# Performance work log

Measured on AMD Instinct MI355X. Metric: run time of the kernel, lower is better.

## Reference

```python
import jax, jax.numpy as jnp
import numpy as np

D_MODEL = 256
NHEAD = 8
AGG = 4
NPE = (832.0, 832.0, 832.0, 832.0)
LAYER_NAMES = ['self', 'cross'] * 4


def layer_norm(x, g, b, eps=1e-5):
    mu = x.mean(-1, keepdims=True)
    var = ((x - mu) ** 2).mean(-1, keepdims=True)
    return (x - mu) * jax.lax.rsqrt(var + eps) * g + b


def rope_tables(h, w, d_model=D_MODEL):
    # i/j positions start at 1 (torch cumsum of ones); npe train/test scaling
    i = (jnp.arange(1, h + 1, dtype=jnp.float32) * (NPE[0] / NPE[2]))[:, None, None]
    j = (jnp.arange(1, w + 1, dtype=jnp.float32) * (NPE[1] / NPE[3]))[None, :, None]
    d4 = d_model // 4
    div = jnp.exp(jnp.arange(d4, dtype=jnp.float32) * (-np.log(10000.0) / d4))

    def interleave(a, bb):
        a = jnp.broadcast_to(a, (h, w, d4))
        bb = jnp.broadcast_to(bb, (h, w, d4))
        return jnp.stack([a, bb], -1).reshape(h, w, 2 * d4)

    sin = interleave(jnp.sin(i * div), jnp.sin(j * div))
    cos = interleave(jnp.cos(i * div), jnp.cos(j * div))
    return jnp.repeat(sin, 2, axis=-1), jnp.repeat(cos, 2, axis=-1)  # [h,w,d_model]


def rotate_half(x):
    xp = x.reshape(*x.shape[:-1], -1, 2)
    return jnp.stack([-xp[..., 1], xp[..., 0]], -1).reshape(*x.shape)


def apply_rope(x, sin, cos):  # x: [b,h,w,c]
    return x * cos + rotate_half(x) * sin


def encoder_layer(x, source, p, use_rope):
    bs, C, H0, W0 = x.shape
    # depthwise-conv aggregation of query features (stride=kernel=AGG, no bias)
    q = jax.lax.conv_general_dilated(
        x, p['agg_w'], (AGG, AGG), 'VALID',
        dimension_numbers=('NCHW', 'OIHW', 'NCHW'), feature_group_count=C)
    q = layer_norm(q.transpose(0, 2, 3, 1), p['ln1_g'], p['ln1_b'])  # [b,h,w,C]
    # max-pool aggregation of source features
    s = jax.lax.reduce_window(source, -jnp.inf, jax.lax.max,
                              (1, 1, AGG, AGG), (1, 1, AGG, AGG), 'VALID')
    s = layer_norm(s.transpose(0, 2, 3, 1), p['ln1_g'], p['ln1_b'])
    query = q @ p['qw']
    key = s @ p['kw']
    value = s @ p['vw']
    if use_rope:
        sin_q, cos_q = rope_tables(query.shape[1], query.shape[2])
        query = apply_rope(query, sin_q, cos_q)
        sin_k, cos_k = rope_tables(key.shape[1], key.shape[2])
        key = apply_rope(key, sin_k, cos_k)
    L = query.shape[1] * query.shape[2]
    S = key.shape[1] * key.shape[2]
    dh = C // NHEAD
    qh = query.reshape(bs, L, NHEAD, dh)
    kh = key.reshape(bs, S, NHEAD, dh)
    vh = value.reshape(bs, S, NHEAD, dh)
    scores = jnp.einsum('blhd,bshd->bhls', qh, kh) / jnp.asarray(dh, qh.dtype) ** 0.5
    attn = jax.nn.softmax(scores, axis=-1)
    m = jnp.einsum('bhls,bshd->blhd', attn, vh).reshape(bs, L, C)
    m = m @ p['mw']  # merge
    m = m.reshape(bs, H0 // AGG, W0 // AGG, C).transpose(0, 3, 1, 2)
    # bilinear upsample x4, align_corners=False (half-pixel, matches jax.image)
    m = jax.image.resize(m, (bs, C, H0, W0), method='bilinear')
    cat = jnp.concatenate([x, m], axis=1).transpose(0, 2, 3, 1)  # [b,H,W,2C]
    h1 = cat @ p['w1']
    h1 = jnp.where(h1 >= 0, h1, 0.01 * h1)  # LeakyReLU
    out = layer_norm(h1 @ p['w2'], p['ln2_g'], p['ln2_b']).transpose(0, 3, 1, 2)
    return x + out


def _forward(feat0, feat1, params):
    for i, name in enumerate(LAYER_NAMES):
        p = {k: v[i] for k, v in params.items()}
        if name == 'self':
            feat0 = encoder_layer(feat0, feat0, p, use_rope=True)
            feat1 = encoder_layer(feat1, feat1, p, use_rope=True)
        else:
            feat0 = encoder_layer(feat0, feat1, p, use_rope=False)
            feat1 = encoder_layer(feat1, feat0, p, use_rope=False)
    return feat0, feat1


def setup_inputs() -> dict:
    key = jax.random.key(0)
    ks = jax.random.split(key, 10)
    C = D_MODEL
    NL = len(LAYER_NAMES)

    def xavier(k, shape, fan_in, fan_out):
        return jax.random.normal(k, shape, jnp.float32) * np.sqrt(2.0 / (fan_in + fan_out))

    return {
        'feat0': jax.random.normal(ks[0], (2, C, 96, 96), jnp.float32),
        'feat1': jax.random.normal(ks[1], (2, C, 96, 96), jnp.float32),
        'agg_w': jax.random.normal(ks[2], (NL, C, 1, AGG, AGG), jnp.float32) * 0.1,
        'qw': xavier(ks[3], (NL, C, C), C, C),
        'kw': xavier(ks[4], (NL, C, C), C, C),
        'vw': xavier(ks[5], (NL, C, C), C, C),
        'mw': xavier(ks[6], (NL, C, C), C, C),
        'w1': xavier(ks[7], (NL, 2 * C, 2 * C), 2 * C, 2 * C),
        'w2': xavier(ks[8], (NL, 2 * C, C), 2 * C, C),
        'ln1_g': jnp.ones((NL, C), jnp.float32),
        'ln1_b': jnp.zeros((NL, C), jnp.float32),
        'ln2_g': jnp.ones((NL, C), jnp.float32),
        'ln2_b': jnp.zeros((NL, C), jnp.float32),
    }


def reference(feat0, feat1, agg_w, qw, kw, vw, mw, w1, w2, ln1_g, ln1_b, ln2_g, ln2_b):
    params = dict(agg_w=agg_w, qw=qw, kw=kw, vw=vw, mw=mw, w1=w1, w2=w2,
                  ln1_g=ln1_g, ln1_b=ln1_b, ln2_g=ln2_g, ln2_b=ln2_b)
    return _forward(feat0, feat1, params)
```

## Files before the change

kernel.cpp:

```cpp
#include <hip/hip_runtime.h>
#include <math.h>

constexpr int BSZ = 2;
constexpr int CH  = 256;
constexpr int IH  = 96, IW = 96;
constexpr int HSS = 24, WSS = 24;
constexpr int SL  = HSS * WSS;
constexpr int NHD = 8, DHD = 32;
constexpr int CH2 = 512;
constexpr int PIX = IH * IW;
constexpr int MFFN = BSZ * PIX;
constexpr long FEATN = (long)BSZ * PIX * CH;

typedef __attribute__((ext_vector_type(8))) short bf16x8;
typedef __attribute__((ext_vector_type(4))) float f32x4;
typedef _Float16 f16;
typedef __attribute__((ext_vector_type(8))) _Float16 f16x8;
typedef __attribute__((ext_vector_type(4))) _Float16 f16x4;


__device__ inline unsigned short f2bf(float f) {
  unsigned u = __float_as_uint(f);
  u += 0x7FFFu + ((u >> 16) & 1u);
  return (unsigned short)(u >> 16);
}
__device__ inline float bf2f(unsigned short u) {
  return __uint_as_float((unsigned)u << 16);
}

__device__ inline void gload16(const void* g, void* l) {
  __builtin_amdgcn_global_load_lds(
      (const __attribute__((address_space(1))) unsigned int*)g,
      (__attribute__((address_space(3))) unsigned int*)l, 16, 0, 0);
}

__global__ __launch_bounds__(256) void k_in_tr(const float* __restrict__ in,
                                               float* __restrict__ out,
                                               unsigned short* __restrict__ outb) {
  __shared__ float t[32][33];
  const int b = blockIdx.z;
  const int p0 = blockIdx.x * 32, c0 = blockIdx.y * 32;
  const int tx = threadIdx.x & 31, ty = threadIdx.x >> 5;
#pragma unroll
  for (int r = 0; r < 4; ++r)
    t[tx][ty + r * 8] = in[((long)b * CH + c0 + ty + r * 8) * PIX + p0 + tx];
  __syncthreads();
#pragma unroll
  for (int r = 0; r < 4; ++r) {
    float v = t[ty + r * 8][tx];
    long row = (long)b * PIX + p0 + ty + r * 8;
    out[row * CH + c0 + tx] = v;
    outb[row * CH + ((c0 + tx) ^ (ty << 3))] = f2bf(v);
  }
}

__global__ __launch_bounds__(256) void k_out_tr(const float* __restrict__ in,
                                                float* __restrict__ out) {
  __shared__ float t[32][33];
  const int b = blockIdx.z;
  const int p0 = blockIdx.x * 32, c0 = blockIdx.y * 32;
  const int tx = threadIdx.x & 31, ty = threadIdx.x >> 5;
#pragma unroll
  for (int r = 0; r < 4; ++r)
    t[ty + r * 8][tx] = in[((long)b * PIX + p0 + ty + r * 8) * CH + c0 + tx];
  __syncthreads();
#pragma unroll
  for (int r = 0; r < 4; ++r)
    out[((long)b * CH + c0 + ty + r * 8) * PIX + p0 + tx] = t[tx][ty + r * 8];
}

__global__ __launch_bounds__(256) void k_wt(const float* __restrict__ W,
                                            unsigned short* __restrict__ WT,
                                            int K, int N, long strideW, long strideT) {
  const long z = blockIdx.z;
  W  += z * strideW;
  WT += z * strideT;
  __shared__ float t[32][33];
  const int n0 = blockIdx.x * 32, k0 = blockIdx.y * 32;
  const int tx = threadIdx.x & 31, ty = threadIdx.x >> 5;
#pragma unroll
  for (int r = 0; r < 4; ++r)
    t[ty + r * 8][tx] = W[(long)(k0 + ty + r * 8) * N + n0 + tx];
  __syncthreads();
#pragma unroll
  for (int r = 0; r < 4; ++r) {
    int n = n0 + ty + r * 8;
    WT[(long)n * K + ((k0 + tx) ^ ((n & 7) << 3))] = f2bf(t[tx][ty + r * 8]);
  }
}

__global__ __launch_bounds__(256) void k_cvt(const float* __restrict__ W,
                                             unsigned short* __restrict__ O) {
  const int i = blockIdx.x;
  const long z = blockIdx.y;
  const int k = threadIdx.x;
  O[(z * CH + i) * CH + (k ^ ((i & 7) << 3))] = f2bf(W[(z * CH + i) * CH + k]);
}

__global__ __launch_bounds__(256) void k_rope_tables(float* __restrict__ sinT,
                                                     float* __restrict__ cosT) {
  int l = blockIdx.x;
  int d = threadIdx.x;
  int ii = l / WSS + 1;
  int jj = l % WSS + 1;
  int kidx = d >> 2;
  bool is_i = ((d >> 1) & 1) == 0;
  float div = expf((float)kidx * -0.14391156831212787f);
  float pos = is_i ? (float)ii : (float)jj;
  float ang = pos * div;
  sinT[(long)l * CH + d] = sinf(ang);
  cosT[(long)l * CH + d] = cosf(ang);
}

__global__ __launch_bounds__(256) void k_agg(const unsigned short* __restrict__ x,
                                             const unsigned short* __restrict__ src,
                                             const float* __restrict__ aggw,
                                             const float* __restrict__ g,
                                             const float* __restrict__ bt,
                                             unsigned short* __restrict__ qln,
                                             unsigned short* __restrict__ sln,
                                             int nb) {
  int bi = blockIdx.x;
  int mode = 0;
  if (bi >= nb * SL) { mode = 1; bi -= nb * SL; }
  int b = bi / SL, l = bi % SL;
  int i = l / WSS, j = l % WSS;
  int c = threadIdx.x;
  const unsigned short* in = mode ? src : x;
  float v;
  if (mode == 0) {
    v = 0.f;
#pragma unroll
    for (int r = 0; r < 4; ++r)
#pragma unroll
      for (int s = 0; s < 4; ++s)
        v += bf2f(in[(((long)b * IH + i * 4 + r) * IW + j * 4 + s) * CH +
                     (c ^ (((j * 4 + s) & 7) << 3))]) *
             aggw[c * 16 + r * 4 + s];
  } else {
    v = -INFINITY;
#pragma unroll
    for (int r = 0; r < 4; ++r)
#pragma unroll
      for (int s = 0; s < 4; ++s)
        v = fmaxf(v, bf2f(in[(((long)b * IH + i * 4 + r) * IW + j * 4 + s) * CH +
                             (c ^ (((j * 4 + s) & 7) << 3))]));
  }
  __shared__ float red[8];
  float s1 = v, s2 = v * v;
#pragma unroll
  for (int d = 1; d < 64; d <<= 1) { s1 += __shfl_xor(s1, d); s2 += __shfl_xor(s2, d); }
  int wv = threadIdx.x >> 6;
  if ((threadIdx.x & 63) == 0) { red[wv * 2] = s1; red[wv * 2 + 1] = s2; }
  __syncthreads();
  s1 = red[0] + red[2] + red[4] + red[6];
  s2 = red[1] + red[3] + red[5] + red[7];
  float mu = s1 * (1.f / CH);
  float var = s2 * (1.f / CH) - mu * mu;
  float o = (v - mu) * rsqrtf(var + 1e-5f) * g[c] + bt[c];
  (mode ? sln : qln)[(long)(b * SL + l) * CH + (c ^ ((l & 7) << 3))] = f2bf(o);
}

template <int BM, int BN, int OUT>
__global__ __launch_bounds__(256) void k_mm(const unsigned short* __restrict__ A,
                                            const unsigned short* __restrict__ A2,
                                            const unsigned short* __restrict__ Bt,
                                            void* __restrict__ C0, void* __restrict__ C1,
                                            void* __restrict__ C2,
                                            int M, int K, int lda, int ldb,
                                            int koffA, int koffB, int ldc,
                                            const float* __restrict__ sinT,
                                            const float* __restrict__ cosT,
                                            long zsA, long zsB, long zsC) {
  constexpr int BK = 64;
  constexpr int WM = BM / 2, WN = BN / 2;
  constexpr int FM = WM / 16, FN = WN / 16;
  constexpr int RA = BM * BK / 2048, RB = BN * BK / 2048;
  __shared__ unsigned short As[2][BM * BK];
  __shared__ unsigned short Bs[2][BN * BK];
  const int tid = threadIdx.x;
  const int lane = tid & 63, w = tid >> 6;
  const int wr = w >> 1, wc = w & 1;
  const int lq = lane & 15, g = lane >> 4;
  const int sw = (lq & 7) << 3;
  const int bm = blockIdx.x * BM, bn = blockIdx.y * BN;
  const long z = blockIdx.z;
  const unsigned short* Ap = ((OUT == 4 && bn >= CH) ? A2 : A) + z * zsA + koffA;
  const unsigned short* Bp = Bt + z * zsB + koffB;

  auto stA = [&](int buf, int k0) {
#pragma unroll
    for (int i = 0; i < RA; ++i) {
      int e = (i * 256 + tid) * 8;
      gload16(Ap + (size_t)(bm + (e >> 6)) * lda + k0 + (e & 63), &As[buf][e]);
    }
  };
  auto stB = [&](int buf, int k0) {
#pragma unroll
    for (int i = 0; i < RB; ++i) {
      int e = (i * 256 + tid) * 8;
      gload16(Bp + (size_t)(bn + (e >> 6)) * ldb + k0 + (e & 63), &Bs[buf][e]);
    }
  };

  f32x4 acc[FM][FN] = {};
  stA(0, 0); stB(0, 0);
  asm volatile("s_waitcnt vmcnt(0)" ::: "memory");
  __syncthreads();
  int cur = 0;
  for (int k0 = 0; k0 < K; k0 += BK) {
    if (k0 + BK < K) { stA(cur ^ 1, k0 + BK); stB(cur ^ 1, k0 + BK); }
#pragma unroll
    for (int ks = 0; ks < 2; ++ks) {
      const int kx = (ks * 32 + g * 8) ^ sw;
      bf16x8 a[FM], b[FN];
#pragma unroll
      for (int m = 0; m < FM; ++m)
        a[m] = *(const bf16x8*)&As[cur][(wr * WM + m * 16 + lq) * BK + kx];
#pragma unroll
      for (int n = 0; n < FN; ++n)
        b[n] = *(const bf16x8*)&Bs[cur][(wc * WN + n * 16 + lq) * BK + kx];
#pragma unroll
      for (int m = 0; m < FM; ++m)
#pragma unroll
        for (int n = 0; n < FN; ++n)
          acc[m][n] = __builtin_amdgcn_mfma_f32_16x16x32_bf16(a[m], b[n], acc[m][n], 0, 0, 0);
    }
    __syncthreads();
    cur ^= 1;
  }
#pragma unroll
  for (int m = 0; m < FM; ++m) {
    const int rowb = bm + wr * WM + m * 16 + g * 4;
#pragma unroll
    for (int n = 0; n < FN; ++n) {
      const int col = bn + wc * WN + n * 16 + lq;
#pragma unroll
      for (int r = 0; r < 4; ++r) {
        const int row = rowb + r;
        float v = acc[m][n][r];
        if (OUT == 0) {
          ((float*)C0 + z * zsC)[(size_t)row * ldc + col] = v;
        } else if (OUT == 5) {
          ((unsigned short*)C0 + z * zsC)[(size_t)row * ldc + (col ^ ((row & 7) << 3))] = f2bf(v);
        } else {
          const int b = row / SL, s = row - b * SL;
          const int which = col >> 8;
          const int ch = col & 255;
          float vp = __shfl_xor(v, 1);
          if (which < 2 && sinT) {
            float sn = sinT[(size_t)s * CH + ch];
            float cs = cosT[(size_t)s * CH + ch];
            v = ((lane & 1) == 0) ? v * cs - vp * sn : v * cs + vp * sn;
          }
          if (which == 0) v *= 0.17677669529663687f;
          const int h = ch >> 5, d = ch & 31;
          if (which == 0)
            ((f16*)C0)[(((size_t)b * NHD + h) * SL + s) * DHD + d] = (f16)v;
          else if (which == 1)
            ((f16*)C1)[(((size_t)b * NHD + h) * SL + s) * DHD + d] = (f16)v;
          else
            ((f16*)C2)[(((size_t)b * NHD + h) * DHD + d) * SL + s] = (f16)v;
        }
      }
    }
  }
}

__global__ __launch_bounds__(64) void k_attn(const f16* __restrict__ qh,
                                             const f16* __restrict__ kh,
                                             const f16* __restrict__ vt,
                                             unsigned short* __restrict__ msgA) {
  const int bh = blockIdx.x;
  const int b = bh >> 3, h = bh & 7;
  const int lane = threadIdx.x;
  const int lq = lane & 15, g = lane >> 4;
  const int q0 = blockIdx.y * 16;

  const f16x8 qf = *(const f16x8*)&qh[((size_t)bh * SL + q0 + lq) * DHD + g * 8];
  const f16* kbase = kh + (size_t)bh * SL * DHD;
  const f16* vbase = vt + (size_t)bh * DHD * SL;

  f16x8 kf = *(const f16x8*)&kbase[(size_t)lq * DHD + g * 8];
  f16x4 va = *(const f16x4*)&vbase[(size_t)lq * SL + g * 4];
  f16x4 vb = *(const f16x4*)&vbase[(size_t)(16 + lq) * SL + g * 4];

  f32x4 o0 = {}, o1 = {};
  float m = -1e30f, l = 0.f;
  for (int t = 0; t < 36; ++t) {
    const int tn = t < 35 ? t + 1 : 35;
    f16x8 kfn = *(const f16x8*)&kbase[((size_t)(tn * 16 + lq)) * DHD + g * 8];
    f16x4 van = *(const f16x4*)&vbase[(size_t)lq * SL + tn * 16 + g * 4];
    f16x4 vbn = *(const f16x4*)&vbase[(size_t)(16 + lq) * SL + tn * 16 + g * 4];
    f32x4 s = __builtin_amdgcn_mfma_f32_16x16x32_f16(kf, qf, (f32x4){0.f, 0.f, 0.f, 0.f}, 0, 0, 0);
    float tm = fmaxf(fmaxf(s[0], s[1]), fmaxf(s[2], s[3]));
    tm = fmaxf(tm, __shfl_xor(tm, 16));
    tm = fmaxf(tm, __shfl_xor(tm, 32));
    if (__any(tm > m + 5.f)) {
      float mn = fmaxf(m, tm);
      float f = __expf(m - mn);
      o0 *= f; o1 *= f; l *= f; m = mn;
    }
    float e0 = __expf(s[0] - m), e1 = __expf(s[1] - m);
    float e2 = __expf(s[2] - m), e3 = __expf(s[3] - m);
    l += (e0 + e1) + (e2 + e3);
    f16x4 ef = {(f16)e0, (f16)e1, (f16)e2, (f16)e3};
    o0 = __builtin_amdgcn_mfma_f32_16x16x16f16(va, ef, o0, 0, 0, 0);
    o1 = __builtin_amdgcn_mfma_f32_16x16x16f16(vb, ef, o1, 0, 0, 0);
    kf = kfn; va = van; vb = vbn;
  }
  l += __shfl_xor(l, 16);
  l += __shfl_xor(l, 32);
  float inv = 1.f / l;
  const int swz = (lq & 7) << 3;
  unsigned short* mrow = msgA + ((size_t)(b * SL + q0 + lq)) * CH;
#pragma unroll
  for (int mt = 0; mt < 2; ++mt) {
    f32x4 o = mt ? o1 : o0;
    unsigned a0 = f2bf(o[0] * inv) | ((unsigned)f2bf(o[1] * inv) << 16);
    unsigned a1 = f2bf(o[2] * inv) | ((unsigned)f2bf(o[3] * inv) << 16);
    uint2 u; u.x = a0; u.y = a1;
    *(uint2*)&mrow[(h * DHD + mt * 16 + g * 4) ^ swz] = u;
  }
}

__global__ __launch_bounds__(256) void k_ffn1(const unsigned short* __restrict__ xb,
                                              const unsigned short* __restrict__ w1T,
                                              const float* __restrict__ Z,
                                              unsigned short* __restrict__ h1) {
  constexpr int BM = 64, BN = 128, BK = 64, K = 256;
  constexpr int WM = 32, WN = 64, FM = 2, FN = 4;
  __shared__ unsigned short As[2][BM * BK];
  __shared__ unsigned short Bs[BN * BK];
  const int tid = threadIdx.x;
  const int lane = tid & 63, w = tid >> 6;
  const int wr = w >> 1, wc = w & 1;
  const int lq = lane & 15, g = lane >> 4;
  const int sw = (lq & 7) << 3;
  const int bm = blockIdx.x * BM, bn = blockIdx.y * BN;

  auto stA = [&](int buf, int k0) {
#pragma unroll
    for (int i = 0; i < 2; ++i) {
      int e = (i * 256 + tid) * 8;
      gload16(xb + (size_t)(bm + (e >> 6)) * 256 + k0 + (e & 63), &As[buf][e]);
    }
  };
  auto stB = [&](int k0) {
#pragma unroll
    for (int i = 0; i < 4; ++i) {
      int e = (i * 256 + tid) * 8;
      gload16(w1T + (size_t)(bn + (e >> 6)) * 512 + k0 + (e & 63), &Bs[e]);
    }
  };

  f32x4 acc[FM][FN] = {};
  stA(0, 0); stB(0);
  asm volatile("s_waitcnt vmcnt(0)" ::: "memory");
  __syncthreads();
  int cur = 0;
  for (int k0 = 0; k0 < K; k0 += BK) {
    if (k0 + BK < K) stA(cur ^ 1, k0 + BK);
#pragma unroll
    for (int ks = 0; ks < 2; ++ks) {
      const int kx = (ks * 32 + g * 8) ^ sw;
      bf16x8 a[FM], b[FN];
#pragma unroll
      for (int m = 0; m < FM; ++m)
        a[m] = *(const bf16x8*)&As[cur][(wr * WM + m * 16 + lq) * BK + kx];
#pragma unroll
      for (int n = 0; n < FN; ++n)
        b[n] = *(const bf16x8*)&Bs[(wc * WN + n * 16 + lq) * BK + kx];
#pragma unroll
      for (int m = 0; m < FM; ++m)
#pragma unroll
        for (int n = 0; n < FN; ++n)
          acc[m][n] = __builtin_amdgcn_mfma_f32_16x16x32_bf16(a[m], b[n], acc[m][n], 0, 0, 0);
    }
    __syncthreads();
    if (k0 + BK < K) stB(k0 + BK);
    asm volatile("s_waitcnt vmcnt(0)" ::: "memory");
    __syncthreads();
    cur ^= 1;
  }
#pragma unroll
  for (int m = 0; m < FM; ++m) {
    const int rowb = bm + wr * WM + m * 16 + g * 4;
#pragma unroll
    for (int r = 0; r < 4; ++r) {
      const int row = rowb + r;
      const int b = row / PIX;
      const int p = row - b * PIX;
      const int y = p / IW, xx = p - y * IW;
      float sy = (y + 0.5f) * 0.25f - 0.5f;
      float sx = (xx + 0.5f) * 0.25f - 0.5f;
      int y0 = (int)floorf(sy); float wy = sy - y0;
      int x0 = (int)floorf(sx); float wx = sx - x0;
      int y1 = min(y0 + 1, HSS - 1); y0 = max(y0, 0);
      int x1 = min(x0 + 1, WSS - 1); x0 = max(x0, 0);
      const float* Zb = Z + (size_t)b * SL * CH2;
      const float* z00 = Zb + (size_t)(y0 * WSS + x0) * CH2;
      const float* z01 = Zb + (size_t)(y0 * WSS + x1) * CH2;
      const float* z10 = Zb + (size_t)(y1 * WSS + x0) * CH2;
      const float* z11 = Zb + (size_t)(y1 * WSS + x1) * CH2;
      float w00 = (1.f - wy) * (1.f - wx), w01 = (1.f - wy) * wx;
      float w10 = wy * (1.f - wx), w11 = wy * wx;
      const int rs = (row & 7) << 3;
#pragma unroll
      for (int n = 0; n < FN; ++n) {
        const int col = bn + wc * WN + n * 16 + lq;
        float v = acc[m][n][r] + w00 * z00[col] + w01 * z01[col] +
                  w10 * z10[col] + w11 * z11[col];
        v = v >= 0.f ? v : 0.01f * v;
        h1[(size_t)row * CH2 + (col ^ rs)] = f2bf(v);
      }
    }
  }
}

__global__ __launch_bounds__(256) void k_ffn2(const unsigned short* __restrict__ A,
                                              const unsigned short* __restrict__ Bt,
                                              const float* __restrict__ g2,
                                              const float* __restrict__ b2,
                                              float* __restrict__ x,
                                              unsigned short* __restrict__ xb) {
  constexpr int BM = 32, BK = 64, K = 512;
  __shared__ unsigned short As[2][BM * BK];
  __shared__ unsigned short Bs[256 * BK];
  __shared__ float sS[2][BM], sQ[2][BM];
  __shared__ float gS[256], bS[256];
  const int tid = threadIdx.x;
  const int lane = tid & 63, w = tid >> 6;
  const int wr = w >> 1, wc = w & 1;
  const int lq = lane & 15, g = lane >> 4;
  const int sw = (lq & 7) << 3;
  const int bm = blockIdx.x * BM;
  gS[tid] = g2[tid]; bS[tid] = b2[tid];

  auto stA = [&](int buf, int k0) {
    int e = tid * 8;
    gload16(A + (size_t)(bm + (e >> 6)) * K + k0 + (e & 63), &As[buf][e]);
  };
  auto stB = [&](int k0) {
#pragma unroll
    for (int i = 0; i < 8; ++i) {
      int e = (i * 256 + tid) * 8;
      gload16(Bt + (size_t)(e >> 6) * K + k0 + (e & 63), &Bs[e]);
    }
  };

  f32x4 acc[8] = {};
  stA(0, 0); stB(0);
  asm volatile("s_waitcnt vmcnt(0)" ::: "memory");
  __syncthreads();
  int cur = 0;
  for (int k0 = 0; k0 < K; k0 += BK) {
    if (k0 + BK < K) stA(cur ^ 1, k0 + BK);
#pragma unroll
    for (int ks = 0; ks < 2; ++ks) {
      const int kx = (ks * 32 + g * 8) ^ sw;
      bf16x8 a = *(const bf16x8*)&As[cur][(wr * 16 + lq) * BK + kx];
      bf16x8 b[8];
#pragma unroll
      for (int n = 0; n < 8; ++n)
        b[n] = *(const bf16x8*)&Bs[(wc * 128 + n * 16 + lq) * BK + kx];
#pragma unroll
      for (int n = 0; n < 8; ++n)
        acc[n] = __builtin_amdgcn_mfma_f32_16x16x32_bf16(a, b[n], acc[n], 0, 0, 0);
    }
    __syncthreads();
    if (k0 + BK < K) stB(k0 + BK);
    asm volatile("s_waitcnt vmcnt(0)" ::: "memory");
    __syncthreads();
    cur ^= 1;
  }
#pragma unroll
  for (int r = 0; r < 4; ++r) {
    float s1 = 0.f, s2 = 0.f;
#pragma unroll
    for (int n = 0; n < 8; ++n) {
      float v = acc[n][r];
      s1 += v; s2 += v * v;
    }
#pragma unroll
    for (int d = 1; d < 16; d <<= 1) {
      s1 += __shfl_xor(s1, d);
      s2 += __shfl_xor(s2, d);
    }
    if (lq == 0) {
      int row = wr * 16 + g * 4 + r;
      sS[wc][row] = s1; sQ[wc][row] = s2;
    }
  }
  __syncthreads();
#pragma unroll
  for (int r = 0; r < 4; ++r) {
    int row = wr * 16 + g * 4 + r;
    float mu = (sS[0][row] + sS[1][row]) * (1.f / CH);
    float var = (sQ[0][row] + sQ[1][row]) * (1.f / CH) - mu * mu;
    float rs = rsqrtf(var + 1e-5f);
    size_t gr = (size_t)(bm + row) * CH;
    const int swr = ((bm + row) & 7) << 3;
#pragma unroll
    for (int n = 0; n < 8; ++n) {
      int col = wc * 128 + n * 16 + lq;
      float o = (acc[n][r] - mu) * rs * gS[col] + bS[col];
      float nx = x[gr + col] + o;
      x[gr + col] = nx;
      xb[gr + (col ^ swr)] = f2bf(nx);
    }
  }
}

struct LayerP {
  const float *aggw, *g1, *b1, *g2, *b2;
  const unsigned short *qkvT, *w1T, *w2T, *wcT;
};

struct Bufs {
  unsigned short *qln, *sln, *msgA, *h1, *xb;
  f16 *qh, *kh, *vt;
  float *Zbuf, *f;
  const float *sinT, *cosT;
};

static void attn_part(long xoff, long soff, const LayerP& p, bool rope, int nb,
                      const Bufs& B, hipStream_t stream) {
  const int M = nb * SL;
  k_agg<<<dim3(2 * nb * SL), 256, 0, stream>>>(B.xb + xoff, B.xb + soff, p.aggw,
                                               p.g1, p.b1, B.qln, B.sln, nb);
  const float* sT = rope ? B.sinT : nullptr;
  const float* cT = rope ? B.cosT : nullptr;
  k_mm<32, 64, 4><<<dim3(M / 32, 12), 256, 0, stream>>>(
      B.qln, B.sln, p.qkvT, B.qh, B.kh, B.vt, M, CH, CH, CH, 0, 0, 0, sT, cT, 0, 0, 0);
  k_attn<<<dim3(nb * NHD, 36), 64, 0, stream>>>(B.qh, B.kh, B.vt, B.msgA);
  k_mm<64, 64, 0><<<dim3(M / 64, 8), 256, 0, stream>>>(
      B.msgA, nullptr, p.wcT, B.Zbuf, nullptr, nullptr, M, CH, CH, CH, 0, 0, CH2,
      nullptr, nullptr, 0, 0, 0);
}

static void ffn_part(int fi, int nf, const float* Zs, const LayerP& p, const Bufs& B,
                     hipStream_t stream) {
  const int M = nf * MFFN;
  k_ffn1<<<dim3(M / 64, CH2 / 128), 256, 0, stream>>>(B.xb + (long)fi * FEATN, p.w1T, Zs, B.h1);
  k_ffn2<<<dim3(M / 32), 256, 0, stream>>>(B.h1, p.w2T, p.g2, p.b2,
                                           B.f + (long)fi * FEATN, B.xb + (long)fi * FEATN);
}

extern "C" void kernel_launch(void* const* d_in, const int* in_sizes, int n_in,
                              void* d_out, int out_size, void* d_ws, size_t ws_size,
                              hipStream_t stream) {
  const float* in_f0 = (const float*)d_in[0];
  const float* in_f1 = (const float*)d_in[1];
  const float* aggw  = (const float*)d_in[2];
  const float* qw    = (const float*)d_in[3];
  const float* kw    = (const float*)d_in[4];
  const float* vw    = (const float*)d_in[5];
  const float* mw    = (const float*)d_in[6];
  const float* w1    = (const float*)d_in[7];
  const float* w2    = (const float*)d_in[8];
  const float* g1    = (const float*)d_in[9];
  const float* b1    = (const float*)d_in[10];
  const float* g2    = (const float*)d_in[11];
  const float* b2    = (const float*)d_in[12];
  (void)in_sizes; (void)n_in; (void)out_size; (void)ws_size;

  char* cur = (char*)d_ws;
  auto alloc = [&](size_t bytes) { void* p = cur; cur += (bytes + 255) & ~(size_t)255; return p; };
  float*          f    = (float*)alloc((size_t)2 * FEATN * 4);
  unsigned short* xb   = (unsigned short*)alloc((size_t)2 * FEATN * 2);
  unsigned short* h1   = (unsigned short*)alloc((size_t)2 * MFFN * CH2 * 2);
  float*          Zbuf = (float*)alloc((size_t)4 * SL * CH2 * 4);
  unsigned short* msgA = (unsigned short*)alloc((size_t)4 * SL * CH * 2);
  unsigned short* qln  = (unsigned short*)alloc((size_t)4 * SL * CH * 2);
  unsigned short* sln  = (unsigned short*)alloc((size_t)4 * SL * CH * 2);
  f16* qh = (f16*)alloc((size_t)4 * NHD * SL * DHD * 2);
  f16* kh = (f16*)alloc((size_t)4 * NHD * SL * DHD * 2);
  f16* vt = (f16*)alloc((size_t)4 * NHD * SL * DHD * 2);
  float* sinT = (float*)alloc((size_t)SL * CH * 4);
  float* cosT = (float*)alloc((size_t)SL * CH * 4);
  unsigned short* qkvT = (unsigned short*)alloc((size_t)8 * 3 * CH * CH * 2);
  unsigned short* mwB  = (unsigned short*)alloc((size_t)8 * CH * CH * 2);
  unsigned short* w1T  = (unsigned short*)alloc((size_t)8 * CH2 * CH2 * 2);
  unsigned short* w2T  = (unsigned short*)alloc((size_t)8 * CH * CH2 * 2);
  unsigned short* wcT  = (unsigned short*)alloc((size_t)8 * CH2 * CH * 2);

  k_in_tr<<<dim3(PIX / 32, CH / 32, BSZ), 256, 0, stream>>>(in_f0, f, xb);
  k_in_tr<<<dim3(PIX / 32, CH / 32, BSZ), 256, 0, stream>>>(in_f1, f + FEATN, xb + FEATN);
  k_rope_tables<<<dim3(SL), 256, 0, stream>>>(sinT, cosT);
  k_wt<<<dim3(CH / 32, CH / 32, 8), 256, 0, stream>>>(qw, qkvT, CH, CH, (long)CH * CH, (long)3 * CH * CH);
  k_wt<<<dim3(CH / 32, CH / 32, 8), 256, 0, stream>>>(kw, qkvT + (size_t)CH * CH, CH, CH, (long)CH * CH, (long)3 * CH * CH);
  k_wt<<<dim3(CH / 32, CH / 32, 8), 256, 0, stream>>>(vw, qkvT + (size_t)2 * CH * CH, CH, CH, (long)CH * CH, (long)3 * CH * CH);
  k_cvt<<<dim3(CH, 8), 256, 0, stream>>>(mw, mwB);
  k_wt<<<dim3(CH2 / 32, CH2 / 32, 8), 256, 0, stream>>>(w1, w1T, CH2, CH2, (long)CH2 * CH2, (long)CH2 * CH2);
  k_wt<<<dim3(CH / 32, CH2 / 32, 8), 256, 0, stream>>>(w2, w2T, CH2, CH, (long)CH2 * CH, (long)CH * CH2);
  k_mm<64, 64, 5><<<dim3(CH2 / 64, CH / 64, 8), 256, 0, stream>>>(
      w1T, nullptr, mwB, wcT, nullptr, nullptr, CH2, CH, CH2, CH, 256, 0, CH,
      nullptr, nullptr, (long)CH2 * CH2, (long)CH * CH, (long)CH2 * CH);

  Bufs B{qln, sln, msgA, h1, xb, qh, kh, vt, Zbuf, f, sinT, cosT};

  for (int i = 0; i < 8; ++i) {
    LayerP p{aggw + (long)i * CH * 16,
             g1 + i * CH, b1 + i * CH, g2 + i * CH, b2 + i * CH,
             qkvT + (long)i * 3 * CH * CH,
             w1T + (long)i * CH2 * CH2, w2T + (long)i * CH * CH2,
             wcT + (long)i * CH2 * CH};
    if ((i & 1) == 0) {
      attn_part(0, 0, p, true, 4, B, stream);
      ffn_part(0, 2, Zbuf, p, B, stream);
    } else {
      attn_part(0, FEATN, p, false, 2, B, stream);
      ffn_part(0, 1, Zbuf, p, B, stream);
      attn_part(FEATN, 0, p, false, 2, B, stream);
      ffn_part(1, 1, Zbuf, p, B, stream);
    }
  }

  float* outp = (float*)d_out;
  k_out_tr<<<dim3(PIX / 32, CH / 32, BSZ), 256, 0, stream>>>(f, outp);
  k_out_tr<<<dim3(PIX / 32, CH / 32, BSZ), 256, 0, stream>>>(f + FEATN, outp + FEATN);
}
```

Before: 1.028 ms.

## Split attention keys across two waves and enlarge FFN GEMM row tiles

The attention kernel now runs two wavefronts per block, each handling half of the key tiles, and merges their partial softmax max, sum and outputs through shared memory. This halves the serial loop length per query tile. Separately, the FFN1 and FFN2 GEMMs double their row tile (64→128 and 32→64) so each weight tile loaded into shared memory is reused over more rows. The larger tiles use more LDS and registers per block and produce fewer blocks, which may reduce occupancy.

```diff
diff --git a/kernel.cpp b/kernel.cpp
--- a/kernel.cpp
+++ b/kernel.cpp
@@ -267,28 +267,32 @@
   }
 }
 
-__global__ __launch_bounds__(64) void k_attn(const f16* __restrict__ qh,
-                                             const f16* __restrict__ kh,
-                                             const f16* __restrict__ vt,
-                                             unsigned short* __restrict__ msgA) {
+__global__ __launch_bounds__(128) void k_attn(const f16* __restrict__ qh,
+                                              const f16* __restrict__ kh,
+                                              const f16* __restrict__ vt,
+                                              unsigned short* __restrict__ msgA) {
   const int bh = blockIdx.x;
   const int b = bh >> 3, h = bh & 7;
-  const int lane = threadIdx.x;
+  const int tid = threadIdx.x;
+  const int sid = tid >> 6;
+  const int lane = tid & 63;
   const int lq = lane & 15, g = lane >> 4;
   const int q0 = blockIdx.y * 16;
 
   const f16x8 qf = *(const f16x8*)&qh[((size_t)bh * SL + q0 + lq) * DHD + g * 8];
   const f16* kbase = kh + (size_t)bh * SL * DHD;
   const f16* vbase = vt + (size_t)bh * DHD * SL;
-
-  f16x8 kf = *(const f16x8*)&kbase[(size_t)lq * DHD + g * 8];
-  f16x4 va = *(const f16x4*)&vbase[(size_t)lq * SL + g * 4];
-  f16x4 vb = *(const f16x4*)&vbase[(size_t)(16 + lq) * SL + g * 4];
+  const int t0 = sid * 18;
+
+  f16x8 kf = *(const f16x8*)&kbase[((size_t)(t0 * 16 + lq)) * DHD + g * 8];
+  f16x4 va = *(const f16x4*)&vbase[(size_t)lq * SL + t0 * 16 + g * 4];
+  f16x4 vb = *(const f16x4*)&vbase[(size_t)(16 + lq) * SL + t0 * 16 + g * 4];
 
   f32x4 o0 = {}, o1 = {};
   float m = -1e30f, l = 0.f;
-  for (int t = 0; t < 36; ++t) {
-    const int tn = t < 35 ? t + 1 : 35;
+  for (int tt = 0; tt < 18; ++tt) {
+    const int t = t0 + tt;
+    const int tn = tt < 17 ? t + 1 : t;
     f16x8 kfn = *(const f16x8*)&kbase[((size_t)(tn * 16 + lq)) * DHD + g * 8];
     f16x4 van = *(const f16x4*)&vbase[(size_t)lq * SL + tn * 16 + g * 4];
     f16x4 vbn = *(const f16x4*)&vbase[(size_t)(16 + lq) * SL + tn * 16 + g * 4];
@@ -311,25 +315,39 @@
   }
   l += __shfl_xor(l, 16);
   l += __shfl_xor(l, 32);
-  float inv = 1.f / l;
+
+  __shared__ float mS[2][16], lS[2][16];
+  __shared__ float oS[2][2][16][17];
+  if (g == 0) { mS[sid][lq] = m; lS[sid][lq] = l; }
+#pragma unroll
+  for (int r = 0; r < 4; ++r) {
+    oS[sid][0][g * 4 + r][lq] = o0[r];
+    oS[sid][1][g * 4 + r][lq] = o1[r];
+  }
+  __syncthreads();
+  float m0 = mS[0][lq], m1 = mS[1][lq];
+  float l0 = lS[0][lq], l1 = lS[1][lq];
+  float mn = fmaxf(m0, m1);
+  float f0 = __expf(m0 - mn), f1 = __expf(m1 - mn);
+  float inv = 1.f / (l0 * f0 + l1 * f1);
+  float ov[4];
+#pragma unroll
+  for (int r = 0; r < 4; ++r)
+    ov[r] = (oS[0][sid][g * 4 + r][lq] * f0 + oS[1][sid][g * 4 + r][lq] * f1) * inv;
   const int swz = (lq & 7) << 3;
   unsigned short* mrow = msgA + ((size_t)(b * SL + q0 + lq)) * CH;
-#pragma unroll
-  for (int mt = 0; mt < 2; ++mt) {
-    f32x4 o = mt ? o1 : o0;
-    unsigned a0 = f2bf(o[0] * inv) | ((unsigned)f2bf(o[1] * inv) << 16);
-    unsigned a1 = f2bf(o[2] * inv) | ((unsigned)f2bf(o[3] * inv) << 16);
-    uint2 u; u.x = a0; u.y = a1;
-    *(uint2*)&mrow[(h * DHD + mt * 16 + g * 4) ^ swz] = u;
-  }
+  unsigned a0 = f2bf(ov[0]) | ((unsigned)f2bf(ov[1]) << 16);
+  unsigned a1 = f2bf(ov[2]) | ((unsigned)f2bf(ov[3]) << 16);
+  uint2 u; u.x = a0; u.y = a1;
+  *(uint2*)&mrow[(h * DHD + sid * 16 + g * 4) ^ swz] = u;
 }
 
 __global__ __launch_bounds__(256) void k_ffn1(const unsigned short* __restrict__ xb,
                                               const unsigned short* __restrict__ w1T,
                                               const float* __restrict__ Z,
                                               unsigned short* __restrict__ h1) {
-  constexpr int BM = 64, BN = 128, BK = 64, K = 256;
-  constexpr int WM = 32, WN = 64, FM = 2, FN = 4;
+  constexpr int BM = 128, BN = 128, BK = 64, K = 256;
+  constexpr int WM = 64, WN = 64, FM = 4, FN = 4;
   __shared__ unsigned short As[2][BM * BK];
   __shared__ unsigned short Bs[BN * BK];
   const int tid = threadIdx.x;
@@ -341,7 +359,7 @@
 
   auto stA = [&](int buf, int k0) {
 #pragma unroll
-    for (int i = 0; i < 2; ++i) {
+    for (int i = 0; i < 4; ++i) {
       int e = (i * 256 + tid) * 8;
       gload16(xb + (size_t)(bm + (e >> 6)) * 256 + k0 + (e & 63), &As[buf][e]);
     }
@@ -424,7 +442,8 @@
                                               const float* __restrict__ b2,
                                               float* __restrict__ x,
                                               unsigned short* __restrict__ xb) {
-  constexpr int BM = 32, BK = 64, K = 512;
+  constexpr int BM = 64, BK = 64, K = 512;
+  constexpr int WM = 32, FM = 2;
   __shared__ unsigned short As[2][BM * BK];
   __shared__ unsigned short Bs[256 * BK];
   __shared__ float sS[2][BM], sQ[2][BM];
@@ -438,8 +457,11 @@
   gS[tid] = g2[tid]; bS[tid] = b2[tid];
 
   auto stA = [&](int buf, int k0) {
-    int e = tid * 8;
-    gload16(A + (size_t)(bm + (e >> 6)) * K + k0 + (e & 63), &As[buf][e]);
+#pragma unroll
+    for (int i = 0; i < 2; ++i) {
+      int e = (i * 256 + tid) * 8;
+      gload16(A + (size_t)(bm + (e >> 6)) * K + k0 + (e & 63), &As[buf][e]);
+    }
   };
   auto stB = [&](int k0) {
 #pragma unroll
@@ -449,7 +471,7 @@
     }
   };
 
-  f32x4 acc[8] = {};
+  f32x4 acc[FM][8] = {};
   stA(0, 0); stB(0);
   asm volatile("s_waitcnt vmcnt(0)" ::: "memory");
   __syncthreads();
@@ -459,14 +481,19 @@
 #pragma unroll
     for (int ks = 0; ks < 2; ++ks) {
       const int kx = (ks * 32 + g * 8) ^ sw;
-      bf16x8 a = *(const bf16x8*)&As[cur][(wr * 16 + lq) * BK + kx];
+      bf16x8 a[FM];
+#pragma unroll
+      for (int m = 0; m < FM; ++m)
+        a[m] = *(const bf16x8*)&As[cur][(wr * WM + m * 16 + lq) * BK + kx];
       bf16x8 b[8];
 #pragma unroll
       for (int n = 0; n < 8; ++n)
         b[n] = *(const bf16x8*)&Bs[(wc * 128 + n * 16 + lq) * BK + kx];
 #pragma unroll
-      for (int n = 0; n < 8; ++n)
-        acc[n] = __builtin_amdgcn_mfma_f32_16x16x32_bf16(a, b[n], acc[n], 0, 0, 0);
+      for (int m = 0; m < FM; ++m)
+#pragma unroll
+        for (int n = 0; n < 8; ++n)
+          acc[m][n] = __builtin_amdgcn_mfma_f32_16x16x32_bf16(a[m], b[n], acc[m][n], 0, 0, 0);
     }
     __syncthreads();
     if (k0 + BK < K) stB(k0 + BK);
@@ -475,41 +502,45 @@
     cur ^= 1;
   }
 #pragma unroll
-  for (int r = 0; r < 4; ++r) {
-    float s1 = 0.f, s2 = 0.f;
-#pragma unroll
-    for (int n = 0; n < 8; ++n) {
-      float v = acc[n][r];
-      s1 += v; s2 += v * v;
-    }
-#pragma unroll
-    for (int d = 1; d < 16; d <<= 1) {
-      s1 += __shfl_xor(s1, d);
-      s2 += __shfl_xor(s2, d);
-    }
-    if (lq == 0) {
-      int row = wr * 16 + g * 4 + r;
-      sS[wc][row] = s1; sQ[wc][row] = s2;
-    }
-  }
-  __syncthreads();
-#pragma unroll
-  for (int r = 0; r < 4; ++r) {
-    int row = wr * 16 + g * 4 + r;
-    float mu = (sS[0][row] + sS[1][row]) * (1.f / CH);
-    float var = (sQ[0][row] + sQ[1][row]) * (1.f / CH) - mu * mu;
-    float rs = rsqrtf(var + 1e-5f);
-    size_t gr = (size_t)(bm + row) * CH;
-    const int swr = ((bm + row) & 7) << 3;
-#pragma unroll
-    for (int n = 0; n < 8; ++n) {
-      int col = wc * 128 + n * 16 + lq;
-      float o = (acc[n][r] - mu) * rs * gS[col] + bS[col];
-      float nx = x[gr + col] + o;
-      x[gr + col] = nx;
-      xb[gr + (col ^ swr)] = f2bf(nx);
-    }
-  }
+  for (int m = 0; m < FM; ++m)
+#pragma unroll
+    for (int r = 0; r < 4; ++r) {
+      float s1 = 0.f, s2 = 0.f;
+#pragma unroll
+      for (int n = 0; n < 8; ++n) {
+        float v = acc[m][n][r];
+        s1 += v; s2 += v * v;
+      }
+#pragma unroll
+      for (int d = 1; d < 16; d <<= 1) {
+        s1 += __shfl_xor(s1, d);
+        s2 += __shfl_xor(s2, d);
+      }
+      if (lq == 0) {
+        int row = wr * WM + m * 16 + g * 4 + r;
+        sS[wc][row] = s1; sQ[wc][row] = s2;
+      }
+    }
+  __syncthreads();
+#pragma unroll
+  for (int m = 0; m < FM; ++m)
+#pragma unroll
+    for (int r = 0; r < 4; ++r) {
+      int row = wr * WM + m * 16 + g * 4 + r;
+      float mu = (sS[0][row] + sS[1][row]) * (1.f / CH);
+      float var = (sQ[0][row] + sQ[1][row]) * (1.f / CH) - mu * mu;
+      float rs = rsqrtf(var + 1e-5f);
+      size_t gr = (size_t)(bm + row) * CH;
+      const int swr = ((bm + row) & 7) << 3;
+#pragma unroll
+      for (int n = 0; n < 8; ++n) {
+        int col = wc * 128 + n * 16 + lq;
+        float o = (acc[m][n][r] - mu) * rs * gS[col] + bS[col];
+        float nx = x[gr + col] + o;
+        x[gr + col] = nx;
+        xb[gr + (col ^ swr)] = f2bf(nx);
+      }
+    }
 }
 
 struct LayerP {
@@ -533,7 +564,7 @@
   const float* cT = rope ? B.cosT : nullptr;
   k_mm<32, 64, 4><<<dim3(M / 32, 12), 256, 0, stream>>>(
       B.qln, B.sln, p.qkvT, B.qh, B.kh, B.vt, M, CH, CH, CH, 0, 0, 0, sT, cT, 0, 0, 0);
-  k_attn<<<dim3(nb * NHD, 36), 64, 0, stream>>>(B.qh, B.kh, B.vt, B.msgA);
+  k_attn<<<dim3(nb * NHD, 36), 128, 0, stream>>>(B.qh, B.kh, B.vt, B.msgA);
   k_mm<64, 64, 0><<<dim3(M / 64, 8), 256, 0, stream>>>(
       B.msgA, nullptr, p.wcT, B.Zbuf, nullptr, nullptr, M, CH, CH, CH, 0, 0, CH2,
       nullptr, nullptr, 0, 0, 0);
@@ -542,8 +573,8 @@
 static void ffn_part(int fi, int nf, const float* Zs, const LayerP& p, const Bufs& B,
                      hipStream_t stream) {
   const int M = nf * MFFN;
-  k_ffn1<<<dim3(M / 64, CH2 / 128), 256, 0, stream>>>(B.xb + (long)fi * FEATN, p.w1T, Zs, B.h1);
-  k_ffn2<<<dim3(M / 32), 256, 0, stream>>>(B.h1, p.w2T, p.g2, p.b2,
+  k_ffn1<<<dim3(M / 128, CH2 / 128), 256, 0, stream>>>(B.xb + (long)fi * FEATN, p.w1T, Zs, B.h1);
+  k_ffn2<<<dim3(M / 64), 256, 0, stream>>>(B.h1, p.w2T, p.g2, p.b2,
                                            B.f + (long)fi * FEATN, B.xb + (long)fi * FEATN);
 }
 
```

Measured after the change: 1.111 ms. 8.0% more time.
